# Kernel optimization log

Measured on AMD Instinct MI355X. Metric: run time of the kernel, lower is better.

Reference implementation:

```python
import jax, jax.numpy as jnp
import numpy as np


def setup_inputs() -> dict:
    key = jax.random.key(0)
    k_x, k_pos, k_val, k_temp = jax.random.split(key, 4)
    B, T, D, N = 8, 2048, 512, 4096
    x = jax.random.normal(k_x, (B, T, D), dtype=jnp.float32)
    # module init: positions ~ N(0,1)*0.5, values ~ N(0,1)*0.02
    positions = jax.random.normal(k_pos, (N, D), dtype=jnp.float32) * 0.5
    values = jax.random.normal(k_val, (N, D), dtype=jnp.float32) * 0.02
    # 'trained' temperatures ~ U[4,6] so the RBF kernel does not underflow at D=512
    temperature = 4.0 + 2.0 * jax.random.uniform(k_temp, (N,), dtype=jnp.float32)
    # neuron_scale buffer at late-tide level (MAX_SCALE = 0.8)
    neuron_scale = jnp.full((N,), 0.8, dtype=jnp.float32)
    return {"x": x, "positions": positions, "values": values,
            "temperature": temperature, "neuron_scale": neuron_scale}


def reference(x, positions, values, temperature, neuron_scale):
    B, T, D = x.shape
    x_flat = x.reshape(-1, D)                                  # [M, D], M = B*T
    x_sq = jnp.sum(x_flat * x_flat, axis=-1, keepdims=True)    # [M, 1]
    p_sq = jnp.sum(positions * positions, axis=-1)             # [N]
    cross = x_flat @ positions.T                               # [M, N] GEMM
    dists = jnp.sqrt(jnp.maximum(x_sq + p_sq[None, :] - 2.0 * cross, 0.0))
    effective_temp = (jnp.abs(temperature) + 0.1) * neuron_scale  # [N]
    weights = jnp.exp(-dists / effective_temp[None, :])        # [M, N]
    weights = weights / (jnp.sum(weights, axis=-1, keepdims=True) + 1e-8)
    out = weights @ values                                     # [M, D] GEMM
    return out.reshape(B, T, D)
```

## Files before the change

### kernel.cpp

```cpp
#include <hip/hip_runtime.h>
#include <hip/hip_bf16.h>

typedef __attribute__((ext_vector_type(8))) short short8;
typedef __attribute__((ext_vector_type(4))) float f32x4;
typedef __attribute__((ext_vector_type(4))) unsigned short u16x4;

__device__ __forceinline__ unsigned short f2bf(float f) {
  union { float f; unsigned u; } v; v.f = f;
  unsigned r = v.u + 0x7fffu + ((v.u >> 16) & 1u);
  return (unsigned short)(r >> 16);
}

template <int EPI, int WM, int WN, int MI>
__global__ __launch_bounds__(512, 4) void rbf_gemm(
    const unsigned short* __restrict__ A, const unsigned short* __restrict__ Bt,
    int Ncols, int K,
    const float* __restrict__ xsq, const float* __restrict__ psq,
    const float* __restrict__ rtemp, unsigned short* __restrict__ Wout,
    float* __restrict__ part, int Mtot, const float* __restrict__ denin,
    float* __restrict__ outp, int row0, int ldOut) {
  constexpr int BM = WM * MI * 16;
  constexpr int BN = WN * 64;
  constexpr int AITERS = BM / 64;
  constexpr int BITERS = BN / 64;
  constexpr int LOADS = AITERS + BITERS;
  constexpr int ASZ = BM * 64;
  constexpr int HALF = ASZ + BN * 64;
  constexpr int BOUNCE = EPI == 1 ? BM * BN * 2 : BM * BN;
  constexpr int SELEMS = 2 * HALF > BOUNCE ? 2 * HALF : BOUNCE;
  __shared__ __align__(16) unsigned short smem[SELEMS];

  const int t = threadIdx.x;
  const int lane = t & 63, wid = t >> 6;
  const int wm = wid / WN, wn = wid % WN;
  const int lr = lane & 15, lg = lane >> 4;

  const int nb = Ncols / BN;
  const int nwg = gridDim.x;
  int swz = blockIdx.x;
  if ((nwg & 7) == 0) {
    int cpx = nwg >> 3;
    swz = (swz & 7) * cpx + (swz >> 3);
  }
  const int bm = swz / nb, bn = swz - bm * nb;

  const unsigned short* Ab = A + (size_t)bm * BM * K;
  const unsigned short* Bb = Bt + (size_t)bn * BN * K;

  const unsigned short* gA[AITERS];
  const unsigned short* gB[BITERS];
#pragma unroll
  for (int i = 0; i < AITERS; ++i) {
    const int idx = i * 512 + t;
    const int r = idx >> 3, c = idx & 7;
    gA[i] = Ab + (size_t)r * K + ((c ^ (r & 7)) << 3);
  }
#pragma unroll
  for (int i = 0; i < BITERS; ++i) {
    const int idx = i * 512 + t;
    const int r = idx >> 3, c = idx & 7;
    gB[i] = Bb + (size_t)r * K + ((c ^ (r & 7)) << 3);
  }
  const int dwave = wid << 9;

  int offA[MI][2], offB[4][2];
#pragma unroll
  for (int mi = 0; mi < MI; ++mi) {
    const int ar = wm * (MI * 16) + mi * 16 + lr;
#pragma unroll
    for (int ks = 0; ks < 2; ++ks)
      offA[mi][ks] = ar * 64 + ((((ks << 2) | lg) ^ (ar & 7)) << 3);
  }
#pragma unroll
  for (int ni = 0; ni < 4; ++ni) {
    const int br = wn * 64 + ni * 16 + lr;
#pragma unroll
    for (int ks = 0; ks < 2; ++ks)
      offB[ni][ks] = ASZ + br * 64 + ((((ks << 2) | lg) ^ (br & 7)) << 3);
  }

  f32x4 acc[MI][4];
#pragma unroll
  for (int i = 0; i < MI; ++i)
#pragma unroll
    for (int j = 0; j < 4; ++j) acc[i][j] = (f32x4){0.f, 0.f, 0.f, 0.f};

#define STAGE(koff, boff)                                                              \
  do {                                                                                 \
    _Pragma("unroll")                                                                  \
    for (int i = 0; i < AITERS; ++i)                                                   \
      __builtin_amdgcn_global_load_lds(                                                \
          (const __attribute__((address_space(1))) void*)(gA[i] + (koff)),             \
          (__attribute__((address_space(3))) void*)(smem + (boff) + i * 4096 + dwave), \
          16, 0, 0);                                                                   \
    _Pragma("unroll")                                                                  \
    for (int i = 0; i < BITERS; ++i)                                                   \
      __builtin_amdgcn_global_load_lds(                                                \
          (const __attribute__((address_space(1))) void*)(gB[i] + (koff)),             \
          (__attribute__((address_space(3))) void*)(smem + (boff) + ASZ + i * 4096 + dwave), \
          16, 0, 0);                                                                   \
  } while (0)

  STAGE(0, 0);
  unsigned buf = 0;
  const int nsteps = K >> 6;
  for (int s = 0; s < nsteps; ++s) {
    if (s + 1 < nsteps) {
      STAGE((s + 1) << 6, buf ^ HALF);
      asm volatile("s_waitcnt vmcnt(%0)" :: "i"(LOADS) : "memory");
    } else {
      asm volatile("s_waitcnt vmcnt(0)" ::: "memory");
    }
    __builtin_amdgcn_s_barrier();
    const unsigned short* sb = smem + buf;
    __builtin_amdgcn_s_setprio(1);
#pragma unroll
    for (int ks = 0; ks < 2; ++ks) {
      short8 af[MI], bf[4];
#pragma unroll
      for (int mi = 0; mi < MI; ++mi) af[mi] = *(const short8*)&sb[offA[mi][ks]];
#pragma unroll
      for (int ni = 0; ni < 4; ++ni) bf[ni] = *(const short8*)&sb[offB[ni][ks]];
#pragma unroll
      for (int mi = 0; mi < MI; ++mi)
#pragma unroll
        for (int ni = 0; ni < 4; ++ni)
          acc[mi][ni] = __builtin_amdgcn_mfma_f32_16x16x32_bf16(af[mi], bf[ni],
                                                                acc[mi][ni], 0, 0, 0);
    }
    __builtin_amdgcn_s_setprio(0);
    asm volatile("s_waitcnt lgkmcnt(0)" ::: "memory");
    __builtin_amdgcn_s_barrier();
    buf ^= HALF;
  }
#undef STAGE

  if (EPI == 0) {
    float ps[4], rt[4];
#pragma unroll
    for (int ni = 0; ni < 4; ++ni) {
      const int col = bn * BN + wn * 64 + ni * 16 + lr;
      ps[ni] = psq[col];
      rt[ni] = rtemp[col];
    }
    float* slice = part + (size_t)(bn * WN + wn) * Mtot;
#pragma unroll
    for (int mi = 0; mi < MI; ++mi) {
#pragma unroll
      for (int j = 0; j < 4; ++j) {
        const int lrow = wm * (MI * 16) + mi * 16 + lg * 4 + j;
        const int grow = row0 + bm * BM + lrow;
        const float xq = xsq[grow];
        float rsv = 0.f;
#pragma unroll
        for (int ni = 0; ni < 4; ++ni) {
          const int lcol = wn * 64 + ni * 16 + lr;
          float d2 = xq + ps[ni] - 2.0f * acc[mi][ni][j];
          float dist = __builtin_amdgcn_sqrtf(fmaxf(d2, 0.0f));
          float w = __builtin_amdgcn_exp2f(-dist * rt[ni]);
          smem[lrow * BN + (((lcol >> 3) ^ (lrow & 7)) << 3) + (lcol & 7)] = f2bf(w);
          rsv += w;
        }
        rsv += __shfl_xor(rsv, 1);
        rsv += __shfl_xor(rsv, 2);
        rsv += __shfl_xor(rsv, 4);
        rsv += __shfl_xor(rsv, 8);
        if (lr == 0) slice[grow] = rsv;
      }
    }
    __syncthreads();
    constexpr int HB = BN / 8;
#pragma unroll
    for (int i = 0; i < BM * BN / 8 / 512; ++i) {
      const int id = i * 512 + t;
      const int r = id / HB, h = id % HB;
      short8 v = *(const short8*)&smem[r * BN + ((h ^ (r & 7)) << 3)];
      __builtin_nontemporal_store(v,
          (short8*)&Wout[(size_t)(bm * BM + r) * ldOut + bn * BN + h * 8]);
    }
  } else {
    float* smemf = (float*)smem;
#pragma unroll
    for (int mi = 0; mi < MI; ++mi)
#pragma unroll
      for (int j = 0; j < 4; ++j) {
        const int lrow = wm * (MI * 16) + mi * 16 + lg * 4 + j;
#pragma unroll
        for (int ni = 0; ni < 4; ++ni) {
          const int lcol = wn * 64 + ni * 16 + lr;
          smemf[lrow * BN + (((lcol >> 2) ^ (lrow & 7)) << 2) + (lcol & 3)] =
              acc[mi][ni][j];
        }
      }
    __syncthreads();
    constexpr int HB4 = BN / 4;
#pragma unroll
    for (int i = 0; i < BM * BN / 4 / 512; ++i) {
      const int id = i * 512 + t;
      const int r = id / HB4, h = id % HB4;
      const int grow = row0 + bm * BM + r;
      const float rd = 1.0f / (denin[grow] + 1e-8f);
      f32x4 v = *(const f32x4*)&smemf[r * BN + ((h ^ (r & 7)) << 2)];
      v *= rd;
      __builtin_nontemporal_store(v,
          (f32x4*)&outp[(size_t)grow * ldOut + bn * BN + h * 4]);
    }
  }
}

__global__ void reduce_denom(const float* __restrict__ part, float* __restrict__ denom,
                             int Mtot, int row0, int S) {
  const int m = row0 + blockIdx.x * 128 + threadIdx.x;
  float s = 0.f;
  for (int i = 0; i < S; ++i) s += part[(size_t)i * Mtot + m];
  denom[m] = s;
}

__global__ void prep_rows(const float* __restrict__ in, unsigned short* __restrict__ outb,
                          float* __restrict__ sq, int D) {
  const int row = blockIdx.x;
  const int t = threadIdx.x;
  const float4 v = ((const float4*)(in + (size_t)row * D))[t];
  u16x4 o = {f2bf(v.x), f2bf(v.y), f2bf(v.z), f2bf(v.w)};
  *(u16x4*)(outb + (size_t)row * D + t * 4) = o;
  float s = v.x * v.x + v.y * v.y + v.z * v.z + v.w * v.w;
  for (int off = 32; off; off >>= 1) s += __shfl_xor(s, off);
  __shared__ float ws[16];
  if ((t & 63) == 0) ws[t >> 6] = s;
  __syncthreads();
  if (t == 0) {
    float tot = 0.f;
    const int nw = blockDim.x >> 6;
    for (int i = 0; i < nw; ++i) tot += ws[i];
    sq[row] = tot;
  }
}

__global__ void prep_scale(const float* __restrict__ tmp, const float* __restrict__ sc,
                           float* __restrict__ rtemp, int N) {
  const int i = blockIdx.x * blockDim.x + threadIdx.x;
  if (i < N) rtemp[i] = 1.4426950408889634f / ((fabsf(tmp[i]) + 0.1f) * sc[i]);
}

__global__ void prep_vT(const float* __restrict__ vals, unsigned short* __restrict__ vT,
                        int N, int D) {
  __shared__ float tile[32][33];
  const int nt = blockIdx.x, dt = blockIdx.y;
  const int tx = threadIdx.x, ty = threadIdx.y;
#pragma unroll
  for (int i = 0; i < 4; ++i) {
    int r = nt * 32 + ty + i * 8;
    tile[ty + i * 8][tx] = vals[(size_t)r * D + dt * 32 + tx];
  }
  __syncthreads();
#pragma unroll
  for (int i = 0; i < 4; ++i) {
    int d = dt * 32 + ty + i * 8;
    vT[(size_t)d * N + nt * 32 + tx] = f2bf(tile[tx][ty + i * 8]);
  }
}

extern "C" void kernel_launch(void* const* d_in, const int* in_sizes, int n_in,
                              void* d_out, int out_size, void* d_ws, size_t ws_size,
                              hipStream_t stream) {
  const float* x = (const float*)d_in[0];
  const float* pos = (const float*)d_in[1];
  const float* vals = (const float*)d_in[2];
  const float* temp = (const float*)d_in[3];
  const float* nsc = (const float*)d_in[4];
  float* out = (float*)d_out;

  const int N = in_sizes[3];
  const int D = in_sizes[1] / N;
  const int M = in_sizes[0] / D;
  const int S = 2 * (N / 128);

  char* ws = (char*)d_ws;
  size_t off = 0;
  auto alloc = [&](size_t bytes) {
    void* p = ws + off;
    off = (off + bytes + 255) & ~(size_t)255;
    return p;
  };
  unsigned short* xb = (unsigned short*)alloc((size_t)M * D * 2);
  unsigned short* pb = (unsigned short*)alloc((size_t)N * D * 2);
  unsigned short* vT = (unsigned short*)alloc((size_t)D * N * 2);
  float* xsq = (float*)alloc((size_t)M * 4);
  float* psq = (float*)alloc((size_t)N * 4);
  float* rtemp = (float*)alloc((size_t)N * 4);
  float* denom = (float*)alloc((size_t)M * 4);
  float* part = (float*)alloc((size_t)S * M * 4);

  size_t avail = ws_size > off ? ws_size - off : 0;
  long long mc_ll = (long long)(avail / ((size_t)N * 2));
  int Mc = (int)((mc_ll / 128) * 128);
  if (Mc > M) Mc = M;
  if (Mc < 128) Mc = 128;
  unsigned short* W = (unsigned short*)alloc((size_t)Mc * N * 2);

  prep_rows<<<M, D / 4, 0, stream>>>(x, xb, xsq, D);
  prep_rows<<<N, D / 4, 0, stream>>>(pos, pb, psq, D);
  prep_scale<<<(N + 255) / 256, 256, 0, stream>>>(temp, nsc, rtemp, N);
  dim3 tg(N / 32, D / 32);
  prep_vT<<<tg, dim3(32, 8), 0, stream>>>(vals, vT, N, D);

  for (int row0 = 0; row0 < M; row0 += Mc) {
    const int mc = (M - row0) < Mc ? (M - row0) : Mc;
    const int g1 = (mc / 128) * (N / 128);
    rbf_gemm<0, 4, 2, 2><<<g1, 512, 0, stream>>>(xb + (size_t)row0 * D, pb, N, D,
                                                 xsq, psq, rtemp, W, part, M,
                                                 nullptr, nullptr, row0, N);
    reduce_denom<<<mc / 128, 128, 0, stream>>>(part, denom, M, row0, S);
    const int g2 = (mc / 128) * (D / 256);
    rbf_gemm<1, 2, 4, 4><<<g2, 512, 0, stream>>>(W, vT, D, N,
                                                 nullptr, nullptr, nullptr, nullptr,
                                                 part, M, denom, out, row0, D);
  }
}
```

Before: 214.1 us.

## Generalize GEMM pipeline to configurable K-tile and buffer depth; triple-buffer first GEMM

Parameterizes the bf16 MFMA GEMM by K-tile size and number of LDS buffers, generalizing the swizzle, load indexing and wait counts to a multi-stage prefetch ring. The distance GEMM now uses a 32-wide K tile with three buffers, so two stages are in flight, while the value GEMM keeps its original 64/2 setup. It also replaces the nontemporal store of the bf16 weight matrix with a normal store, which may let the second GEMM read W from cache. Smaller K tiles double the number of barriers per K, and the deeper pipeline changes LDS usage, which could affect occupancy.

```diff
diff --git a/kernel.cpp b/kernel.cpp
--- a/kernel.cpp
+++ b/kernel.cpp
@@ -11,7 +11,7 @@
   return (unsigned short)(r >> 16);
 }
 
-template <int EPI, int WM, int WN, int MI>
+template <int EPI, int WM, int WN, int MI, int BK, int NBUF>
 __global__ __launch_bounds__(512, 4) void rbf_gemm(
     const unsigned short* __restrict__ A, const unsigned short* __restrict__ Bt,
     int Ncols, int K,
@@ -21,13 +21,17 @@
     float* __restrict__ outp, int row0, int ldOut) {
   constexpr int BM = WM * MI * 16;
   constexpr int BN = WN * 64;
-  constexpr int AITERS = BM / 64;
-  constexpr int BITERS = BN / 64;
-  constexpr int LOADS = AITERS + BITERS;
-  constexpr int ASZ = BM * 64;
-  constexpr int HALF = ASZ + BN * 64;
+  constexpr int CH = BK / 8;
+  constexpr int CMASK = CH - 1;
+  constexpr int AIT = BM * CH / 512;
+  constexpr int BIT = BN * CH / 512;
+  constexpr int LOADS = AIT + BIT;
+  constexpr int DEPTH = NBUF - 1;
+  constexpr int KS = BK / 32;
+  constexpr int ASZ = BM * BK;
+  constexpr int TSZ = (BM + BN) * BK;
   constexpr int BOUNCE = EPI == 1 ? BM * BN * 2 : BM * BN;
-  constexpr int SELEMS = 2 * HALF > BOUNCE ? 2 * HALF : BOUNCE;
+  constexpr int SELEMS = NBUF * TSZ > BOUNCE ? NBUF * TSZ : BOUNCE;
   __shared__ __align__(16) unsigned short smem[SELEMS];
 
   const int t = threadIdx.x;
@@ -47,36 +51,36 @@
   const unsigned short* Ab = A + (size_t)bm * BM * K;
   const unsigned short* Bb = Bt + (size_t)bn * BN * K;
 
-  const unsigned short* gA[AITERS];
-  const unsigned short* gB[BITERS];
-#pragma unroll
-  for (int i = 0; i < AITERS; ++i) {
+  const unsigned short* gA[AIT];
+  const unsigned short* gB[BIT];
+#pragma unroll
+  for (int i = 0; i < AIT; ++i) {
     const int idx = i * 512 + t;
-    const int r = idx >> 3, c = idx & 7;
-    gA[i] = Ab + (size_t)r * K + ((c ^ (r & 7)) << 3);
-  }
-#pragma unroll
-  for (int i = 0; i < BITERS; ++i) {
+    const int r = idx / CH, c = idx & CMASK;
+    gA[i] = Ab + (size_t)r * K + ((c ^ (r & CMASK)) << 3);
+  }
+#pragma unroll
+  for (int i = 0; i < BIT; ++i) {
     const int idx = i * 512 + t;
-    const int r = idx >> 3, c = idx & 7;
-    gB[i] = Bb + (size_t)r * K + ((c ^ (r & 7)) << 3);
+    const int r = idx / CH, c = idx & CMASK;
+    gB[i] = Bb + (size_t)r * K + ((c ^ (r & CMASK)) << 3);
   }
   const int dwave = wid << 9;
 
-  int offA[MI][2], offB[4][2];
+  int offA[MI][KS], offB[4][KS];
 #pragma unroll
   for (int mi = 0; mi < MI; ++mi) {
     const int ar = wm * (MI * 16) + mi * 16 + lr;
 #pragma unroll
-    for (int ks = 0; ks < 2; ++ks)
-      offA[mi][ks] = ar * 64 + ((((ks << 2) | lg) ^ (ar & 7)) << 3);
+    for (int ks = 0; ks < KS; ++ks)
+      offA[mi][ks] = ar * BK + ((((ks << 2) | lg) ^ (ar & CMASK)) << 3);
   }
 #pragma unroll
   for (int ni = 0; ni < 4; ++ni) {
     const int br = wn * 64 + ni * 16 + lr;
 #pragma unroll
-    for (int ks = 0; ks < 2; ++ks)
-      offB[ni][ks] = ASZ + br * 64 + ((((ks << 2) | lg) ^ (br & 7)) << 3);
+    for (int ks = 0; ks < KS; ++ks)
+      offB[ni][ks] = ASZ + br * BK + ((((ks << 2) | lg) ^ (br & CMASK)) << 3);
   }
 
   f32x4 acc[MI][4];
@@ -85,37 +89,44 @@
 #pragma unroll
     for (int j = 0; j < 4; ++j) acc[i][j] = (f32x4){0.f, 0.f, 0.f, 0.f};
 
-#define STAGE(koff, boff)                                                              \
+#define STAGE(step, bufi)                                                              \
   do {                                                                                 \
+    const int ko = (step) * BK;                                                        \
+    const int bo = (bufi) * TSZ;                                                       \
     _Pragma("unroll")                                                                  \
-    for (int i = 0; i < AITERS; ++i)                                                   \
+    for (int i = 0; i < AIT; ++i)                                                      \
       __builtin_amdgcn_global_load_lds(                                                \
-          (const __attribute__((address_space(1))) void*)(gA[i] + (koff)),             \
-          (__attribute__((address_space(3))) void*)(smem + (boff) + i * 4096 + dwave), \
+          (const __attribute__((address_space(1))) void*)(gA[i] + ko),                 \
+          (__attribute__((address_space(3))) void*)(smem + bo + i * 4096 + dwave),     \
           16, 0, 0);                                                                   \
     _Pragma("unroll")                                                                  \
-    for (int i = 0; i < BITERS; ++i)                                                   \
+    for (int i = 0; i < BIT; ++i)                                                      \
       __builtin_amdgcn_global_load_lds(                                                \
-          (const __attribute__((address_space(1))) void*)(gB[i] + (koff)),             \
-          (__attribute__((address_space(3))) void*)(smem + (boff) + ASZ + i * 4096 + dwave), \
+          (const __attribute__((address_space(1))) void*)(gB[i] + ko),                 \
+          (__attribute__((address_space(3))) void*)(smem + bo + ASZ + i * 4096 + dwave), \
           16, 0, 0);                                                                   \
   } while (0)
 
-  STAGE(0, 0);
-  unsigned buf = 0;
-  const int nsteps = K >> 6;
+  const int nsteps = K / BK;
+#pragma unroll
+  for (int p = 0; p < DEPTH; ++p)
+    if (p < nsteps) STAGE(p, p);
+
+  int bc = 0, bp = DEPTH % NBUF;
   for (int s = 0; s < nsteps; ++s) {
-    if (s + 1 < nsteps) {
-      STAGE((s + 1) << 6, buf ^ HALF);
+    if (s + DEPTH < nsteps) {
+      STAGE(s + DEPTH, bp);
+      asm volatile("s_waitcnt vmcnt(%0)" :: "i"(DEPTH * LOADS) : "memory");
+    } else if (DEPTH >= 2 && s + 1 < nsteps) {
       asm volatile("s_waitcnt vmcnt(%0)" :: "i"(LOADS) : "memory");
     } else {
       asm volatile("s_waitcnt vmcnt(0)" ::: "memory");
     }
     __builtin_amdgcn_s_barrier();
-    const unsigned short* sb = smem + buf;
+    const unsigned short* sb = smem + bc * TSZ;
     __builtin_amdgcn_s_setprio(1);
 #pragma unroll
-    for (int ks = 0; ks < 2; ++ks) {
+    for (int ks = 0; ks < KS; ++ks) {
       short8 af[MI], bf[4];
 #pragma unroll
       for (int mi = 0; mi < MI; ++mi) af[mi] = *(const short8*)&sb[offA[mi][ks]];
@@ -131,7 +142,8 @@
     __builtin_amdgcn_s_setprio(0);
     asm volatile("s_waitcnt lgkmcnt(0)" ::: "memory");
     __builtin_amdgcn_s_barrier();
-    buf ^= HALF;
+    bc = bc + 1 == NBUF ? 0 : bc + 1;
+    bp = bp + 1 == NBUF ? 0 : bp + 1;
   }
 #undef STAGE
 
@@ -175,8 +187,7 @@
       const int id = i * 512 + t;
       const int r = id / HB, h = id % HB;
       short8 v = *(const short8*)&smem[r * BN + ((h ^ (r & 7)) << 3)];
-      __builtin_nontemporal_store(v,
-          (short8*)&Wout[(size_t)(bm * BM + r) * ldOut + bn * BN + h * 8]);
+      *(short8*)&Wout[(size_t)(bm * BM + r) * ldOut + bn * BN + h * 8] = v;
     }
   } else {
     float* smemf = (float*)smem;
@@ -307,13 +318,13 @@
   for (int row0 = 0; row0 < M; row0 += Mc) {
     const int mc = (M - row0) < Mc ? (M - row0) : Mc;
     const int g1 = (mc / 128) * (N / 128);
-    rbf_gemm<0, 4, 2, 2><<<g1, 512, 0, stream>>>(xb + (size_t)row0 * D, pb, N, D,
-                                                 xsq, psq, rtemp, W, part, M,
-                                                 nullptr, nullptr, row0, N);
+    rbf_gemm<0, 4, 2, 2, 32, 3><<<g1, 512, 0, stream>>>(
+        xb + (size_t)row0 * D, pb, N, D, xsq, psq, rtemp, W, part, M,
+        nullptr, nullptr, row0, N);
     reduce_denom<<<mc / 128, 128, 0, stream>>>(part, denom, M, row0, S);
     const int g2 = (mc / 128) * (D / 256);
-    rbf_gemm<1, 2, 4, 4><<<g2, 512, 0, stream>>>(W, vT, D, N,
-                                                 nullptr, nullptr, nullptr, nullptr,
-                                                 part, M, denom, out, row0, D);
-  }
-}
+    rbf_gemm<1, 2, 4, 4, 64, 2><<<g2, 512, 0, stream>>>(
+        W, vT, D, N, nullptr, nullptr, nullptr, nullptr,
+        part, M, denom, out, row0, D);
+  }
+}
```

After: 216.3 us. Within noise of the previous version (+1.0%).
